# Kernel tuning notes

Hardware: AMD Instinct MI355X
Metric: run time of the kernel (lower is better)

## Reference

```python
import jax, jax.numpy as jnp
import numpy as np

N = 50000      # nodes
E = 800000     # edges (avg degree 16)
D = 64         # node_dim == hidden_dim
ED = 16        # edge_dim
L = 3          # num_layers (3 GATv2 convs)
NEG_SLOPE = 0.2
BN_EPS = 1e-5


def setup_inputs() -> dict:
    key = jax.random.key(0)
    ks = jax.random.split(key, 9)
    x = jax.random.normal(ks[0], (N, D), dtype=jnp.float32)
    edge_index = jax.random.randint(ks[1], (2, E), 0, N, dtype=jnp.int64)
    edge_attr = jax.random.normal(ks[2], (E, ED), dtype=jnp.float32)
    s = 1.0 / np.sqrt(D)
    Wl = jax.random.normal(ks[3], (L, D, D), dtype=jnp.float32) * s    # lin_l per layer
    Wr = jax.random.normal(ks[4], (L, D, D), dtype=jnp.float32) * s    # lin_r per layer
    We = jax.random.normal(ks[5], (L, ED, D), dtype=jnp.float32) * (1.0 / np.sqrt(ED))  # lin_edge
    att = jax.random.normal(ks[6], (L, D), dtype=jnp.float32) * s      # attention vector a
    bias = jnp.zeros((L, D), dtype=jnp.float32)
    gamma = jnp.ones((2, D), dtype=jnp.float32)   # 2 BatchNorms actually used
    beta = jnp.zeros((2, D), dtype=jnp.float32)
    return dict(x=x, edge_index=edge_index, edge_attr=edge_attr,
                Wl=Wl, Wr=Wr, We=We, att=att, bias=bias, gamma=gamma, beta=beta)


def _batchnorm(h, g, b):
    mu = jnp.mean(h, axis=0)
    var = jnp.var(h, axis=0)
    return (h - mu) * jax.lax.rsqrt(var + BN_EPS) * g + b


def _gatv2(h, src, dst, ea, Wl, Wr, We, att, bias, n):
    # PyG GATv2Conv (heads=1): x_l = lin_l(x) (source), x_r = lin_r(x) (target)
    xl = h @ Wl                              # [n, D]
    xr = h @ Wr                              # [n, D]
    ee = ea @ We                             # [E+n, D] edge embeddings
    m = xl[src] + xr[dst] + ee               # [E+n, D]
    s = jax.nn.leaky_relu(m, NEG_SLOPE) @ att  # [E+n] attention logits
    # segment softmax over incoming edges per destination node
    smax = jax.ops.segment_max(s, dst, num_segments=n)
    ev = jnp.exp(s - smax[dst])
    denom = jax.ops.segment_sum(ev, dst, num_segments=n)
    alpha = ev / denom[dst]                  # [E+n]
    out = jax.ops.segment_sum(alpha[:, None] * xl[src], dst, num_segments=n)
    return out + bias


def reference(x, edge_index, edge_attr, Wl, Wr, We, att, bias, gamma, beta):
    n = x.shape[0]
    src, dst = edge_index[0], edge_index[1]
    # add self-loops; loop edge_attr = per-target-node mean of incoming edge_attr
    ones = jnp.ones((edge_attr.shape[0],), dtype=x.dtype)
    cnt = jax.ops.segment_sum(ones, dst, num_segments=n)
    loop_attr = jax.ops.segment_sum(edge_attr, dst, num_segments=n) / jnp.maximum(cnt, 1.0)[:, None]
    ar = jnp.arange(n, dtype=src.dtype)
    src_a = jnp.concatenate([src, ar])
    dst_a = jnp.concatenate([dst, ar])
    ea_a = jnp.concatenate([edge_attr, loop_attr], axis=0)

    # conv1 -> ELU -> BN0
    h = _gatv2(x, src_a, dst_a, ea_a, Wl[0], Wr[0], We[0], att[0], bias[0], n)
    h = jax.nn.elu(h)
    h = _batchnorm(h, gamma[0], beta[0])
    # convs[0] (l=0 != num_layers-2): BN1 -> ELU
    h = _gatv2(h, src_a, dst_a, ea_a, Wl[1], Wr[1], We[1], att[1], bias[1], n)
    h = _batchnorm(h, gamma[1], beta[1])
    h = jax.nn.elu(h)
    # convs[1] (l=1 == num_layers-2): no BN/ELU
    h = _gatv2(h, src_a, dst_a, ea_a, Wl[2], Wr[2], We[2], att[2], bias[2], n)
    return h
```

## Files before the change

### kernel.cpp

```cpp
#include <hip/hip_runtime.h>
#include <math.h>

#define D 64
#define ED 16
#define NEG 0.2f
#define BN_EPS 1e-5f


__global__ void k_count(const int* __restrict__ dst, int* __restrict__ cnt,
                        float* __restrict__ stat, int e) {
    int i = blockIdx.x * blockDim.x + threadIdx.x;
    if (blockIdx.x == 0 && threadIdx.x < 256) stat[threadIdx.x] = 0.f;
    if (i < e) atomicAdd(&cnt[dst[i]], 1);
}

__global__ void k_scan1(const int* __restrict__ cnt, int* __restrict__ off,
                        int* __restrict__ bsum, int n) {
    __shared__ int buf[1024];
    int i = blockIdx.x * 1024 + threadIdx.x;
    int v = (i < n) ? cnt[i] : 0;
    buf[threadIdx.x] = v;
    __syncthreads();
    for (int d = 1; d < 1024; d <<= 1) {
        int t = (threadIdx.x >= (unsigned)d) ? buf[threadIdx.x - d] : 0;
        __syncthreads();
        buf[threadIdx.x] += t;
        __syncthreads();
    }
    if (i < n) off[i + 1] = buf[threadIdx.x];
    if (threadIdx.x == 1023) bsum[blockIdx.x] = buf[1023];
    if (i == 0) off[0] = 0;
}

__global__ void k_scan2(int* __restrict__ bsum, int nb) {
    int l = threadIdx.x;
    int v = (l < nb) ? bsum[l] : 0;
    #pragma unroll
    for (int o = 1; o < 64; o <<= 1) {
        int t = __shfl_up(v, o, 64);
        if (l >= o) v += t;
    }
    int ex = __shfl_up(v, 1, 64);
    if (l == 0) ex = 0;
    if (l < nb) bsum[l] = ex;
}

__global__ void k_scan3(int* __restrict__ off, const int* __restrict__ bsum, int n) {
    int i = blockIdx.x * blockDim.x + threadIdx.x;
    if (i < n) off[i + 1] += bsum[i >> 10];
}

__global__ void k_part(const int* __restrict__ off, int* __restrict__ wbeg,
                       int n, int nw) {
    int w = blockIdx.x * blockDim.x + threadIdx.x;
    if (w > nw) return;
    const long long C = 6;
    long long total = (long long)off[n] + C * n;
    long long target = (total * w) / nw;
    int lo = 0, hi = n;
    while (lo < hi) {
        int mid = (lo + hi) >> 1;
        long long f = (long long)off[mid] + C * mid;
        if (f < target) lo = mid + 1; else hi = mid;
    }
    wbeg[w] = lo;
}

__global__ void k_scatter(const int* __restrict__ src, const int* __restrict__ dst,
                          const int* __restrict__ off, int* __restrict__ fill,
                          int* __restrict__ srcs, float4* __restrict__ eas4,
                          const float4* __restrict__ ea4, int e) {
    int i = blockIdx.x * blockDim.x + threadIdx.x;
    if (i < e) {
        int d = dst[i];
        int p = off[d] + atomicAdd(&fill[d], 1);
        srcs[p] = src[i];
        size_t qi = 4 * (size_t)i;
        int qp = 4 * p;
        float4 a0 = ea4[qi], a1 = ea4[qi + 1], a2 = ea4[qi + 2], a3 = ea4[qi + 3];
        eas4[qp] = a0; eas4[qp + 1] = a1; eas4[qp + 2] = a2; eas4[qp + 3] = a3;
    }
}


#define BN_ELU_APPLY(v0, v1) { \
    if (mode) { \
        v0.x = v0.x * scs[0] + shs[0]; v0.y = v0.y * scs[1] + shs[1]; \
        v0.z = v0.z * scs[2] + shs[2]; v0.w = v0.w * scs[3] + shs[3]; \
        v1.x = v1.x * scs[4] + shs[4]; v1.y = v1.y * scs[5] + shs[5]; \
        v1.z = v1.z * scs[6] + shs[6]; v1.w = v1.w * scs[7] + shs[7]; \
        if (mode == 2) { \
            v0.x = (v0.x > 0.f) ? v0.x : expm1f(v0.x); \
            v0.y = (v0.y > 0.f) ? v0.y : expm1f(v0.y); \
            v0.z = (v0.z > 0.f) ? v0.z : expm1f(v0.z); \
            v0.w = (v0.w > 0.f) ? v0.w : expm1f(v0.w); \
            v1.x = (v1.x > 0.f) ? v1.x : expm1f(v1.x); \
            v1.y = (v1.y > 0.f) ? v1.y : expm1f(v1.y); \
            v1.z = (v1.z > 0.f) ? v1.z : expm1f(v1.z); \
            v1.w = (v1.w > 0.f) ? v1.w : expm1f(v1.w); \
        } \
    } }

__global__ __launch_bounds__(256) void k_gemm(
        const float* __restrict__ h, const float* __restrict__ Wl,
        const float* __restrict__ Wr, float* __restrict__ xl,
        float* __restrict__ xr, const float* __restrict__ stat,
        const float* __restrict__ gamma, const float* __restrict__ beta,
        int mode, int n) {
    __shared__ float lh[4][512];
    int lane = threadIdx.x & 63;
    int w = threadIdx.x >> 6;
    float wl[D], wr[D];
    #pragma unroll
    for (int k = 0; k < D; ++k) { wl[k] = Wl[k * D + lane]; wr[k] = Wr[k * D + lane]; }
    int srow = lane >> 3, scol = (lane & 7) * 8;
    float scs[8], shs[8];
    #pragma unroll
    for (int j = 0; j < 8; ++j) { scs[j] = 1.f; shs[j] = 0.f; }
    if (mode) {
        #pragma unroll
        for (int j = 0; j < 8; ++j) {
            int c = scol + j;
            float s = stat[c], q = stat[64 + c];
            float mean = s / (float)n;
            float var  = q / (float)n - mean * mean;
            float scv = gamma[c] * rsqrtf(var + BN_EPS);
            scs[j] = scv; shs[j] = beta[c] - mean * scv;
        }
    }
    int wid = blockIdx.x * 4 + w;
    int stride = gridDim.x * 4 * 8;
    int r0 = wid * 8;
    float* lp = &lh[w][srow * 64 + scol];
    if (r0 < n) {
        int r = r0 + srow;
        float4 v0 = make_float4(0.f, 0.f, 0.f, 0.f);
        float4 v1 = make_float4(0.f, 0.f, 0.f, 0.f);
        if (r < n) {
            const float4* hp = (const float4*)(h + (size_t)r * D + scol);
            v0 = hp[0]; v1 = hp[1];
        }
        BN_ELU_APPLY(v0, v1)
        ((float4*)lp)[0] = v0; ((float4*)lp)[1] = v1;
    }
    for (; r0 < n; r0 += stride) {
        int rn = r0 + stride;
        float4 p0 = make_float4(0.f, 0.f, 0.f, 0.f);
        float4 p1 = make_float4(0.f, 0.f, 0.f, 0.f);
        if (rn < n) {
            int r = rn + srow;
            if (r < n) {
                const float4* hp = (const float4*)(h + (size_t)r * D + scol);
                p0 = hp[0]; p1 = hp[1];
            }
        }
        #pragma unroll
        for (int rr = 0; rr < 8; rr += 2) {
            const float4* row0 = (const float4*)&lh[w][rr * 64];
            const float4* row1 = (const float4*)&lh[w][rr * 64 + 64];
            float a0 = 0.f, b0 = 0.f, a1 = 0.f, b1 = 0.f;
            #pragma unroll
            for (int kk = 0; kk < 16; ++kk) {
                float4 h0 = row0[kk];
                float4 h1 = row1[kk];
                a0 += h0.x*wl[4*kk] + h0.y*wl[4*kk+1] + h0.z*wl[4*kk+2] + h0.w*wl[4*kk+3];
                b0 += h0.x*wr[4*kk] + h0.y*wr[4*kk+1] + h0.z*wr[4*kk+2] + h0.w*wr[4*kk+3];
                a1 += h1.x*wl[4*kk] + h1.y*wl[4*kk+1] + h1.z*wl[4*kk+2] + h1.w*wl[4*kk+3];
                b1 += h1.x*wr[4*kk] + h1.y*wr[4*kk+1] + h1.z*wr[4*kk+2] + h1.w*wr[4*kk+3];
            }
            int rA = r0 + rr, rB = rA + 1;
            if (rA < n) { xl[(size_t)rA * D + lane] = a0; xr[(size_t)rA * D + lane] = b0; }
            if (rB < n) { xl[(size_t)rB * D + lane] = a1; xr[(size_t)rB * D + lane] = b1; }
        }
        if (rn < n) {
            BN_ELU_APPLY(p0, p1)
            ((float4*)lp)[0] = p0; ((float4*)lp)[1] = p1;
        }
    }
}


#define EEVB(eb, j0) { \
    float4 u0 = *(const float4*)(lwp + (j0 + 0) * 64); \
    float4 u1 = *(const float4*)(lwp + (j0 + 1) * 64); \
    float4 u2 = *(const float4*)(lwp + (j0 + 2) * 64); \
    float4 u3 = *(const float4*)(lwp + (j0 + 3) * 64); \
    eex += eb.x*u0.x + eb.y*u1.x + eb.z*u2.x + eb.w*u3.x; \
    eey += eb.x*u0.y + eb.y*u1.y + eb.z*u2.y + eb.w*u3.y; \
    eez += eb.x*u0.z + eb.y*u1.z + eb.z*u2.z + eb.w*u3.z; \
    eew += eb.x*u0.w + eb.y*u1.w + eb.z*u2.w + eb.w*u3.w; }

__global__ __launch_bounds__(256) void k_gat(
        const float4* __restrict__ xl4, const float4* __restrict__ xr4,
        const float4* __restrict__ eas4, const int* __restrict__ srcs,
        const int* __restrict__ off, const int* __restrict__ wbeg,
        const float4* __restrict__ We4, const float4* __restrict__ att4,
        const float4* __restrict__ bias4, float* __restrict__ out,
        float* __restrict__ stat, int n, int do_elu) {
    __shared__ float ls[128];
    __shared__ float lwe[1024];
    if (threadIdx.x < 128) ls[threadIdx.x] = 0.f;
    ((float4*)lwe)[threadIdx.x] = We4[threadIdx.x];
    __syncthreads();
    int lane = threadIdx.x & 63;
    int g = lane >> 4, c16 = lane & 15;
    const float* lwp = lwe + c16 * 4;
    float4 av = att4[c16];
    float4 b4 = bias4[c16];
    int wid = blockIdx.x * (blockDim.x >> 6) + (threadIdx.x >> 6);
    int ns = wbeg[wid], nt = wbeg[wid + 1];
    float bsx = 0.f, bsy = 0.f, bsz = 0.f, bsw = 0.f;
    float bqx = 0.f, bqy = 0.f, bqz = 0.f, bqw = 0.f;
    int beg = (ns < nt) ? off[ns] : 0;
    for (int i = ns; i < nt; ++i) {
        int end = off[i + 1];
        int deg = end - beg;
        float4 xrv = xr4[i * 16 + c16];
        float denom = 0.f;
        float ax = 0.f, ay = 0.f, az = 0.f, aw = 0.f;
        float ex = 0.f, ey = 0.f, ez = 0.f, ew = 0.f;
        if (deg > 0) {
            int actc = (g < deg);
            int p = beg + (actc ? g : 0);
            int s0 = srcs[p];
            int q = 4 * p;
            float4 e0 = eas4[q], e1 = eas4[q + 1], e2 = eas4[q + 2], e3 = eas4[q + 3];
            float4 X = xl4[s0 * 16 + c16];
            for (int pos = beg; pos < end; pos += 4) {
                int posn = pos + 4;
                int remn = end - posn;
                int actn = (remn > 0) && (g < remn);
                int pn = (remn > 0) ? posn + (actn ? g : 0) : pos;
                int sn = srcs[pn];
                int qn = 4 * pn;
                float4 ne0 = eas4[qn],     ne1 = eas4[qn + 1];
                float4 ne2 = eas4[qn + 2], ne3 = eas4[qn + 3];
                float eex = 0.f, eey = 0.f, eez = 0.f, eew = 0.f;
                EEVB(e0, 0) EEVB(e1, 4) EEVB(e2, 8) EEVB(e3, 12)
                float4 xn = xl4[sn * 16 + c16];
                float mk = actc ? 1.f : 0.f;
                ex += mk * eex; ey += mk * eey; ez += mk * eez; ew += mk * eew;
                float mx = X.x + xrv.x + eex;
                float my = X.y + xrv.y + eey;
                float mz = X.z + xrv.z + eez;
                float mw = X.w + xrv.w + eew;
                float p0 = fmaxf(mx, NEG * mx) * av.x
                         + fmaxf(my, NEG * my) * av.y
                         + fmaxf(mz, NEG * mz) * av.z
                         + fmaxf(mw, NEG * mw) * av.w;
                #pragma unroll
                for (int o = 1; o <= 8; o <<= 1) p0 += __shfl_xor(p0, o, 64);
                float ev = mk * __expf(p0);
                denom += ev;
                ax += ev * X.x;
                ay += ev * X.y;
                az += ev * X.z;
                aw += ev * X.w;
                e0 = ne0; e1 = ne1; e2 = ne2; e3 = ne3; X = xn; actc = actn;
            }
        }
        #pragma unroll
        for (int o = 16; o <= 32; o <<= 1) {
            denom += __shfl_xor(denom, o, 64);
            ax += __shfl_xor(ax, o, 64);
            ay += __shfl_xor(ay, o, 64);
            az += __shfl_xor(az, o, 64);
            aw += __shfl_xor(aw, o, 64);
            ex += __shfl_xor(ex, o, 64);
            ey += __shfl_xor(ey, o, 64);
            ez += __shfl_xor(ez, o, 64);
            ew += __shfl_xor(ew, o, 64);
        }
        float inv = (deg > 0) ? 1.f / (float)deg : 0.f;
        float4 xli = xl4[i * 16 + c16];
        float mx = xli.x + xrv.x + ex * inv;
        float my = xli.y + xrv.y + ey * inv;
        float mz = xli.z + xrv.z + ez * inv;
        float mw = xli.w + xrv.w + ew * inv;
        float p0 = fmaxf(mx, NEG * mx) * av.x
                 + fmaxf(my, NEG * my) * av.y
                 + fmaxf(mz, NEG * mz) * av.z
                 + fmaxf(mw, NEG * mw) * av.w;
        #pragma unroll
        for (int o = 1; o <= 8; o <<= 1) p0 += __shfl_xor(p0, o, 64);
        float ev = __expf(p0);
        denom += ev;
        ax += ev * xli.x;
        ay += ev * xli.y;
        az += ev * xli.z;
        aw += ev * xli.w;
        float invd = 1.f / denom;
        float ox = ax * invd + b4.x;
        float oy = ay * invd + b4.y;
        float oz = az * invd + b4.z;
        float ow = aw * invd + b4.w;
        if (do_elu) {
            ox = (ox > 0.f) ? ox : expm1f(ox);
            oy = (oy > 0.f) ? oy : expm1f(oy);
            oz = (oz > 0.f) ? oz : expm1f(oz);
            ow = (ow > 0.f) ? ow : expm1f(ow);
        }
        if (g == 0) {
            float4 o4; o4.x = ox; o4.y = oy; o4.z = oz; o4.w = ow;
            ((float4*)out)[i * 16 + c16] = o4;
            if (stat) {
                bsx += ox; bsy += oy; bsz += oz; bsw += ow;
                bqx += ox * ox; bqy += oy * oy; bqz += oz * oz; bqw += ow * ow;
            }
        }
        beg = end;
    }
    if (stat) {
        if (g == 0) {
            atomicAdd(&ls[c16 * 4 + 0], bsx);
            atomicAdd(&ls[c16 * 4 + 1], bsy);
            atomicAdd(&ls[c16 * 4 + 2], bsz);
            atomicAdd(&ls[c16 * 4 + 3], bsw);
            atomicAdd(&ls[64 + c16 * 4 + 0], bqx);
            atomicAdd(&ls[64 + c16 * 4 + 1], bqy);
            atomicAdd(&ls[64 + c16 * 4 + 2], bqz);
            atomicAdd(&ls[64 + c16 * 4 + 3], bqw);
        }
        __syncthreads();
        if (threadIdx.x < 128) atomicAdd(&stat[threadIdx.x], ls[threadIdx.x]);
    }
}


extern "C" void kernel_launch(void* const* d_in, const int* in_sizes, int n_in,
                              void* d_out, int out_size, void* d_ws, size_t ws_size,
                              hipStream_t stream) {
    const float* x     = (const float*)d_in[0];
    const int*   ei    = (const int*)d_in[1];
    const float* ea    = (const float*)d_in[2];
    const float* Wl    = (const float*)d_in[3];
    const float* Wr    = (const float*)d_in[4];
    const float* We    = (const float*)d_in[5];
    const float* att   = (const float*)d_in[6];
    const float* bias  = (const float*)d_in[7];
    const float* gamma = (const float*)d_in[8];
    const float* beta  = (const float*)d_in[9];
    float* out = (float*)d_out;

    int n = in_sizes[0] / D;
    int e = in_sizes[1] / 2;
    const int* src = ei;
    const int* dst = ei + e;
    int nb = (n + 1023) / 1024;

    float* xl   = (float*)d_ws;
    float* xr   = xl + (size_t)n * D;
    float* hbuf = xr + (size_t)n * D;
    float* stat = hbuf + (size_t)n * D;
    float* eas  = stat + 256;
    int* cnt  = (int*)(eas + (size_t)e * ED);
    int* fill = cnt + n;
    int* off  = fill + n;
    int* bsum = off + n + 1;
    int* srcs = bsum + 256;
    int* wbeg = srcs + e;

    const int gat_grid  = 1536;
    const int nw = gat_grid * 4;
    const int gemm_grid = 512;

    hipMemsetAsync(cnt, 0, (size_t)(2 * n) * sizeof(int), stream);
    k_count<<<(e + 255) / 256, 256, 0, stream>>>(dst, cnt, stat, e);
    k_scan1<<<nb, 1024, 0, stream>>>(cnt, off, bsum, n);
    k_scan2<<<1, 64, 0, stream>>>(bsum, nb);
    k_scan3<<<(n + 255) / 256, 256, 0, stream>>>(off, bsum, n);
    k_part<<<(nw + 1 + 255) / 256, 256, 0, stream>>>(off, wbeg, n, nw);
    k_scatter<<<(e + 255) / 256, 256, 0, stream>>>(src, dst, off, fill, srcs,
                                                   (float4*)eas, (const float4*)ea, e);

    k_gemm<<<gemm_grid, 256, 0, stream>>>(x, Wl, Wr, xl, xr, stat, gamma, beta, 0, n);
    k_gat<<<gat_grid, 256, 0, stream>>>((const float4*)xl, (const float4*)xr,
                                        (const float4*)eas, srcs, off, wbeg,
                                        (const float4*)We, (const float4*)att,
                                        (const float4*)bias, hbuf, stat, n, 1);
    k_gemm<<<gemm_grid, 256, 0, stream>>>(hbuf, Wl + D * D, Wr + D * D, xl, xr,
                                          stat, gamma, beta, 1, n);
    k_gat<<<gat_grid, 256, 0, stream>>>((const float4*)xl, (const float4*)xr,
                                        (const float4*)eas, srcs, off, wbeg,
                                        (const float4*)(We + ED * D), (const float4*)(att + D),
                                        (const float4*)(bias + D), hbuf, stat + 128, n, 0);
    k_gemm<<<gemm_grid, 256, 0, stream>>>(hbuf, Wl + 2 * D * D, Wr + 2 * D * D, xl, xr,
                                          stat + 128, gamma + D, beta + D, 2, n);
    k_gat<<<gat_grid, 256, 0, stream>>>((const float4*)xl, (const float4*)xr,
                                        (const float4*)eas, srcs, off, wbeg,
                                        (const float4*)(We + 2 * ED * D), (const float4*)(att + 2 * D),
                                        (const float4*)(bias + 2 * D), out, (float*)nullptr, n, 0);
}
```

Baseline: 599.9 us.

## Fold scan and partition kernels into neighbors, use DPP row reductions

Merges the single-block block-sum scan into the per-element offset fixup kernel, with each block redoing the 64-entry scan in shared memory. The workload-partition binary search moves into the scatter kernel, which cuts two kernel launches from the preprocessing chain. The 16-lane attention-logit reduction in the GAT kernel now uses DPP row operations instead of xor shuffles, and the edge-attribute loads in scatter are issued before the atomic. Each scan3 block repeats the small scan, and the scatter kernel gets a longer tail for threads that also run the binary search.

```diff
diff --git a/kernel.cpp b/kernel.cpp
--- a/kernel.cpp
+++ b/kernel.cpp
@@ -32,52 +32,50 @@
     if (i == 0) off[0] = 0;
 }
 
-__global__ void k_scan2(int* __restrict__ bsum, int nb) {
-    int l = threadIdx.x;
-    int v = (l < nb) ? bsum[l] : 0;
-    #pragma unroll
-    for (int o = 1; o < 64; o <<= 1) {
-        int t = __shfl_up(v, o, 64);
-        if (l >= o) v += t;
-    }
-    int ex = __shfl_up(v, 1, 64);
-    if (l == 0) ex = 0;
-    if (l < nb) bsum[l] = ex;
-}
-
-__global__ void k_scan3(int* __restrict__ off, const int* __restrict__ bsum, int n) {
-    int i = blockIdx.x * blockDim.x + threadIdx.x;
-    if (i < n) off[i + 1] += bsum[i >> 10];
-}
-
-__global__ void k_part(const int* __restrict__ off, int* __restrict__ wbeg,
-                       int n, int nw) {
-    int w = blockIdx.x * blockDim.x + threadIdx.x;
-    if (w > nw) return;
-    const long long C = 6;
-    long long total = (long long)off[n] + C * n;
-    long long target = (total * w) / nw;
-    int lo = 0, hi = n;
-    while (lo < hi) {
-        int mid = (lo + hi) >> 1;
-        long long f = (long long)off[mid] + C * mid;
-        if (f < target) lo = mid + 1; else hi = mid;
-    }
-    wbeg[w] = lo;
+__global__ void k_scan3(int* __restrict__ off, const int* __restrict__ bsum,
+                        int n, int nb) {
+    __shared__ int pfx[64];
+    int t = threadIdx.x;
+    if (t < 64) {
+        int v = (t < nb) ? bsum[t] : 0;
+        #pragma unroll
+        for (int o = 1; o < 64; o <<= 1) {
+            int u = __shfl_up(v, o, 64);
+            if (t >= o) v += u;
+        }
+        int ex = __shfl_up(v, 1, 64);
+        pfx[t] = (t == 0) ? 0 : ex;
+    }
+    __syncthreads();
+    int i = blockIdx.x * blockDim.x + t;
+    if (i < n) off[i + 1] += pfx[i >> 10];
 }
 
 __global__ void k_scatter(const int* __restrict__ src, const int* __restrict__ dst,
                           const int* __restrict__ off, int* __restrict__ fill,
                           int* __restrict__ srcs, float4* __restrict__ eas4,
-                          const float4* __restrict__ ea4, int e) {
+                          const float4* __restrict__ ea4, int e,
+                          int* __restrict__ wbeg, int nwv, int n) {
     int i = blockIdx.x * blockDim.x + threadIdx.x;
+    if (i <= nwv) {
+        const long long C = 6;
+        long long total = (long long)off[n] + C * n;
+        long long target = (total * i) / nwv;
+        int lo = 0, hi = n;
+        while (lo < hi) {
+            int mid = (lo + hi) >> 1;
+            long long f = (long long)off[mid] + C * mid;
+            if (f < target) lo = mid + 1; else hi = mid;
+        }
+        wbeg[i] = lo;
+    }
     if (i < e) {
         int d = dst[i];
+        size_t qi = 4 * (size_t)i;
+        float4 a0 = ea4[qi], a1 = ea4[qi + 1], a2 = ea4[qi + 2], a3 = ea4[qi + 3];
         int p = off[d] + atomicAdd(&fill[d], 1);
         srcs[p] = src[i];
-        size_t qi = 4 * (size_t)i;
         int qp = 4 * p;
-        float4 a0 = ea4[qi], a1 = ea4[qi + 1], a2 = ea4[qi + 2], a3 = ea4[qi + 3];
         eas4[qp] = a0; eas4[qp + 1] = a1; eas4[qp + 2] = a2; eas4[qp + 3] = a3;
     }
 }
@@ -179,6 +177,19 @@
     }
 }
 
+
+template <int CTRL>
+__device__ __forceinline__ float dpp_row_add(float x) {
+    int yi = __builtin_amdgcn_update_dpp(0, __float_as_int(x), CTRL, 0xF, 0xF, true);
+    return x + __int_as_float(yi);
+}
+__device__ __forceinline__ float row16_reduce(float x) {
+    x = dpp_row_add<0xB1>(x);
+    x = dpp_row_add<0x4E>(x);
+    x = dpp_row_add<0x124>(x);
+    x = dpp_row_add<0x128>(x);
+    return x;
+}
 
 #define EEVB(eb, j0) { \
     float4 u0 = *(const float4*)(lwp + (j0 + 0) * 64); \
@@ -248,8 +259,7 @@
                          + fmaxf(my, NEG * my) * av.y
                          + fmaxf(mz, NEG * mz) * av.z
                          + fmaxf(mw, NEG * mw) * av.w;
-                #pragma unroll
-                for (int o = 1; o <= 8; o <<= 1) p0 += __shfl_xor(p0, o, 64);
+                p0 = row16_reduce(p0);
                 float ev = mk * __expf(p0);
                 denom += ev;
                 ax += ev * X.x;
@@ -281,8 +291,7 @@
                  + fmaxf(my, NEG * my) * av.y
                  + fmaxf(mz, NEG * mz) * av.z
                  + fmaxf(mw, NEG * mw) * av.w;
-        #pragma unroll
-        for (int o = 1; o <= 8; o <<= 1) p0 += __shfl_xor(p0, o, 64);
+        p0 = row16_reduce(p0);
         float ev = __expf(p0);
         denom += ev;
         ax += ev * xli.x;
@@ -367,11 +376,10 @@
     hipMemsetAsync(cnt, 0, (size_t)(2 * n) * sizeof(int), stream);
     k_count<<<(e + 255) / 256, 256, 0, stream>>>(dst, cnt, stat, e);
     k_scan1<<<nb, 1024, 0, stream>>>(cnt, off, bsum, n);
-    k_scan2<<<1, 64, 0, stream>>>(bsum, nb);
-    k_scan3<<<(n + 255) / 256, 256, 0, stream>>>(off, bsum, n);
-    k_part<<<(nw + 1 + 255) / 256, 256, 0, stream>>>(off, wbeg, n, nw);
+    k_scan3<<<(n + 255) / 256, 256, 0, stream>>>(off, bsum, n, nb);
     k_scatter<<<(e + 255) / 256, 256, 0, stream>>>(src, dst, off, fill, srcs,
-                                                   (float4*)eas, (const float4*)ea, e);
+                                                   (float4*)eas, (const float4*)ea, e,
+                                                   wbeg, nw, n);
 
     k_gemm<<<gemm_grid, 256, 0, stream>>>(x, Wl, Wr, xl, xr, stat, gamma, beta, 0, n);
     k_gat<<<gat_grid, 256, 0, stream>>>((const float4*)xl, (const float4*)xr,
```

After: 565.6 us. 5.7% less time.
